# Optimization experiments

Measured on AMD Instinct MI355X. Metric: run time of the kernel, lower is better.

## Reference

```python
import jax, jax.numpy as jnp
import numpy as np

B, NS, D, H, L, NQ, NK = 32, 4096, 256, 4, 6, 512, 1024
DH = D // H
SCALE = 1.0 / np.sqrt(DH)


def _ln(x, scale, bias, eps=1e-5):
    m = jnp.mean(x, axis=-1, keepdims=True)
    v = jnp.mean((x - m) ** 2, axis=-1, keepdims=True)
    return (x - m) * jax.lax.rsqrt(v + eps) * scale + bias


def setup_inputs() -> dict:
    key = jax.random.key(0)
    ks = jax.random.split(key, 12)
    d = {
        'update_tensor': jax.random.normal(ks[0], (B, NS, D), jnp.float32) * 0.1,
        'emb_table': jax.random.normal(ks[1], (NS + 1, D), jnp.float32) * 0.1,
        'mask_logits': jax.random.uniform(ks[2], (L, NQ, NK), jnp.float32),
        'Wq': jax.random.normal(ks[3], (D, D), jnp.float32) * 0.05,
        'Wk': jax.random.normal(ks[4], (D, D), jnp.float32) * 0.05,
        'Wv': jax.random.normal(ks[5], (D, D), jnp.float32) * 0.05,
        'Wo': jax.random.normal(ks[6], (D, D), jnp.float32) * 0.05,
        'W1': jax.random.normal(ks[7], (D, D), jnp.float32) * 0.05,
        'b1': jnp.zeros((D,), jnp.float32),
        'W2': jax.random.normal(ks[8], (D, D), jnp.float32) * 0.05,
        'b2': jnp.zeros((D,), jnp.float32),
        'sys_scale': jnp.ones((D,), jnp.float32),
        'sys_bias': jnp.zeros((D,), jnp.float32),
        'eff_scale': jnp.ones((D,), jnp.float32),
        'eff_bias': jnp.zeros((D,), jnp.float32),
        'inner_scale': jnp.ones((D,), jnp.float32),
        'inner_bias': jnp.zeros((D,), jnp.float32),
        'outer_scale': jnp.ones((D,), jnp.float32),
        'outer_bias': jnp.zeros((D,), jnp.float32),
        'query_idx': jax.random.randint(ks[9], (L, NQ), 0, NS).astype(jnp.int32),
        'key_idx': jax.random.randint(ks[10], (L, NK), 0, NS).astype(jnp.int32),
    }
    return d


def _hitr(q, k, mask, Wq, Wk, Wv, Wo, W1, b1, W2, b2, in_s, in_b, out_s, out_b):
    # q: [B,NQ,D] (pre-normed), k: [B,NK,D], mask: [NQ,NK] bool
    Q = jnp.einsum('bqd,de->bqe', q, Wq).reshape(B, NQ, H, DH)
    K = jnp.einsum('bkd,de->bke', k, Wk).reshape(B, NK, H, DH)
    V = jnp.einsum('bkd,de->bke', k, Wv).reshape(B, NK, H, DH)
    scores = jnp.einsum('bqhd,bkhd->bhqk', Q, K) * SCALE
    scores = jnp.where(mask[None, None], scores, jnp.float32(-1e9))
    attn = jax.nn.softmax(scores, axis=-1)
    ctx = jnp.einsum('bhqk,bkhd->bqhd', attn, V).reshape(B, NQ, D)
    h = _ln(jnp.einsum('bqd,de->bqe', ctx, Wo), in_s, in_b)
    ffn = jnp.einsum('bqd,de->bqe', jax.nn.gelu(jnp.einsum('bqd,de->bqe', h, W1) + b1), W2) + b2
    return _ln(h + ffn, out_s, out_b)


def reference(update_tensor, emb_table, mask_logits, Wq, Wk, Wv, Wo, W1, b1, W2, b2,
              sys_scale, sys_bias, eff_scale, eff_bias, inner_scale, inner_bias,
              outer_scale, outer_bias, query_idx, key_idx):
    update_result = jnp.zeros_like(update_tensor)
    for l in range(L):  # static hierarchy levels
        qi, ki = query_idx[l], key_idx[l]
        mask = mask_logits[l] > 0.5
        q = _ln(emb_table[qi][None] + update_tensor[:, qi], sys_scale, sys_bias)
        k = _ln(emb_table[ki][None] + update_tensor[:, ki], sys_scale, sys_bias)
        res = _ln(_hitr(q, k, mask, Wq, Wk, Wv, Wo, W1, b1, W2, b2,
                        inner_scale, inner_bias, outer_scale, outer_bias),
                  eff_scale, eff_bias)
        update_tensor = update_tensor.at[:, qi].add(res)
        update_result = update_result.at[:, qi].add(res)
    return update_result
```

## Files before the change

kernel.cpp:

```cpp
#include <hip/hip_runtime.h>
#include <cstdint>
#include <cstddef>

#define B_ 32
#define NS_ 4096
#define D_ 256
#define H_ 4
#define L_ 6
#define NQ_ 512
#define NK_ 1024
#define DH_ 64
#define SCALE_ 0.125f

typedef unsigned short ushort_t;
typedef unsigned long long u64_t;
typedef __bf16 bf16x8 __attribute__((ext_vector_type(8)));
typedef float f32x4 __attribute__((ext_vector_type(4)));

__device__ __forceinline__ ushort_t f2bf(float f) {
  unsigned u = __float_as_uint(f);
  u += 0x7fffu + ((u >> 16) & 1u);
  return (ushort_t)(u >> 16);
}

__device__ __forceinline__ void gld16(const void* g, void* l) {
  __builtin_amdgcn_global_load_lds(
      (__attribute__((address_space(1))) void*)(uintptr_t)g,
      (__attribute__((address_space(3))) void*)(uintptr_t)l, 16, 0, 0);
}

__device__ __forceinline__ float2 block_sum2(float a, float b) {
  __shared__ float sA[4], sB[4];
#pragma unroll
  for (int o = 32; o; o >>= 1) {
    a += __shfl_xor(a, o);
    b += __shfl_xor(b, o);
  }
  const int w = threadIdx.x >> 6;
  __syncthreads();
  if ((threadIdx.x & 63) == 0) { sA[w] = a; sB[w] = b; }
  __syncthreads();
  return make_float2(sA[0] + sA[1] + sA[2] + sA[3], sB[0] + sB[1] + sB[2] + sB[3]);
}

__global__ __launch_bounds__(256) void prep_w(
    const float* __restrict__ w0, const float* __restrict__ w1,
    const float* __restrict__ w2, const float* __restrict__ w3,
    const float* __restrict__ w4, const float* __restrict__ w5,
    ushort_t* __restrict__ wt) {
  const int sel = blockIdx.x >> 8;
  const int n = blockIdx.x & 255;
  const int k = threadIdx.x;
  const float* W = sel == 0 ? w0 : sel == 1 ? w1 : sel == 2 ? w2
                 : sel == 3 ? w3 : sel == 4 ? w4 : w5;
  wt[sel * 65536 + n * 256 + k] = f2bf(W[k * 256 + n]);
}

__global__ __launch_bounds__(256) void prep_mask(
    const float* __restrict__ ml, u64_t* __restrict__ mb) {
  const long gid = (long)blockIdx.x * 256 + threadIdx.x;
  const bool m = ml[gid] > 0.5f;
  const u64_t bal = __ballot(m);
  if ((threadIdx.x & 63) == 0) mb[gid >> 6] = bal;
}

__global__ __launch_bounds__(256) void gather_ln(
    const float* __restrict__ ut, const float* __restrict__ emb,
    const int* __restrict__ qidx, const int* __restrict__ kidx,
    const float* __restrict__ sc, const float* __restrict__ bi,
    ushort_t* __restrict__ qn, ushort_t* __restrict__ kn) {
  const int r = blockIdx.x;
  const int t = threadIdx.x;
  int bb, idx;
  ushort_t* dst;
  long drow;
  if (r < B_ * NQ_) {
    bb = r >> 9; idx = qidx[r & (NQ_ - 1)]; dst = qn; drow = r;
  } else {
    const int r2 = r - B_ * NQ_;
    bb = r2 >> 10; idx = kidx[r2 & (NK_ - 1)]; dst = kn; drow = r2;
  }
  const float x = emb[(long)idx * 256 + t] + ut[((long)bb * NS_ + idx) * 256 + t];
  const float2 s = block_sum2(x, x * x);
  const float mean = s.x * (1.f / 256.f);
  const float var = s.y * (1.f / 256.f) - mean * mean;
  const float inv = rsqrtf(var + 1e-5f);
  dst[drow * 256 + t] = f2bf((x - mean) * inv * sc[t] + bi[t]);
}

template <int EPI>
__device__ __forceinline__ void gemm_body(
    const ushort_t* __restrict__ A, const ushort_t* __restrict__ Bt,
    const float* __restrict__ bias, void* __restrict__ Cout,
    long m0, int n0, ushort_t* lAB) {
  ushort_t* lA = lAB;
  ushort_t* lB = lAB + 8192;
  const int tid = threadIdx.x;
  const int lane = tid & 63, w = tid >> 6;
  const int quad = lane >> 4, l16 = lane & 15;
  const int wm = w & 1, wn = w >> 1;

  f32x4 acc[4][4] = {};

  for (int kt = 0; kt < 4; ++kt) {
    const int k0 = kt * 64;
#pragma unroll
    for (int p = 0; p < 4; ++p) {
      const int ob = p * 4096 + tid * 16;
      const int row = ob >> 7;
      const int chunk = ((ob >> 4) & 7) ^ (row & 7);
      gld16(A + (m0 + row) * 256 + k0 + chunk * 8, (char*)lA + p * 4096 + w * 1024);
      gld16(Bt + (long)(n0 + row) * 256 + k0 + chunk * 8, (char*)lB + p * 4096 + w * 1024);
    }
    __syncthreads();
#pragma unroll
    for (int ki = 0; ki < 2; ++ki) {
      bf16x8 af[4], bfr[4];
#pragma unroll
      for (int i = 0; i < 4; ++i) {
        const int ra = wm * 64 + i * 16 + l16;
        const int ca = (ki * 4 + quad) ^ (ra & 7);
        af[i] = *(const bf16x8*)&lA[ra * 64 + ca * 8];
        const int rb = wn * 64 + i * 16 + l16;
        const int cb = (ki * 4 + quad) ^ (rb & 7);
        bfr[i] = *(const bf16x8*)&lB[rb * 64 + cb * 8];
      }
#pragma unroll
      for (int mi = 0; mi < 4; ++mi)
#pragma unroll
        for (int ni = 0; ni < 4; ++ni)
          acc[mi][ni] = __builtin_amdgcn_mfma_f32_16x16x32_bf16(af[mi], bfr[ni], acc[mi][ni], 0, 0, 0);
    }
    __syncthreads();
  }

  if (EPI == 4) {
    const long b = m0 >> 10;
    const int kvseg = (int)(m0 & 1023);
#pragma unroll
    for (int hg = 0; hg < 2; ++hg) {
      if (wn == hg) {
#pragma unroll
        for (int mi = 0; mi < 4; ++mi)
#pragma unroll
          for (int ni = 0; ni < 4; ++ni)
#pragma unroll
            for (int r = 0; r < 4; ++r) {
              const int dh = ni * 16 + l16;
              const int kvl = wm * 64 + mi * 16 + quad * 4 + r;
              lAB[dh * 128 + (((kvl >> 3) ^ (dh & 15)) << 3) + (kvl & 7)] =
                  f2bf(acc[mi][ni][r]);
            }
      }
      __syncthreads();
      {
        const int dh = tid >> 2;
        const int head = (n0 >> 6) + hg;
        ushort_t* dst = (ushort_t*)Cout +
            ((b * 4 + head) * 64 + dh) * 1024 + kvseg;
#pragma unroll
        for (int i = 0; i < 4; ++i) {
          const int c = (tid & 3) * 4 + i;
          const int cs = c ^ (dh & 15);
          *(uint4*)(dst + c * 8) = *(const uint4*)&lAB[dh * 128 + cs * 8];
        }
      }
      __syncthreads();
    }
    return;
  }

#pragma unroll
  for (int mi = 0; mi < 4; ++mi) {
#pragma unroll
    for (int ni = 0; ni < 4; ++ni) {
#pragma unroll
      for (int r = 0; r < 4; ++r) {
        const long row = m0 + wm * 64 + mi * 16 + quad * 4 + r;
        const int col = n0 + wn * 64 + ni * 16 + l16;
        float v = acc[mi][ni][r];
        if (EPI == 2 || EPI == 3) v += bias[col];
        if (EPI == 2) {
          const float u = 0.7978845608028654f * (v + 0.044715f * v * v * v);
          v = 0.5f * v * (1.0f + tanhf(u));
        }
        if (EPI == 5) v *= SCALE_;
        if (EPI == 0 || EPI == 2 || EPI == 5)
          ((ushort_t*)Cout)[row * 256 + col] = f2bf(v);
        else
          ((float*)Cout)[row * 256 + col] = v;
      }
    }
  }
}

template <int EPI>
__global__ __launch_bounds__(256) void gemm256(
    const ushort_t* __restrict__ A, const ushort_t* __restrict__ Bt,
    const float* __restrict__ bias, void* __restrict__ Cout) {
  __shared__ ushort_t lAB[16384];
  gemm_body<EPI>(A, Bt, bias, Cout, (long)blockIdx.x * 128, blockIdx.y * 128, lAB);
}

__global__ __launch_bounds__(256) void gemm_qkv(
    const ushort_t* __restrict__ qn, const ushort_t* __restrict__ kn,
    const ushort_t* __restrict__ wt,
    ushort_t* __restrict__ Qb, ushort_t* __restrict__ Kb, ushort_t* __restrict__ Vt) {
  __shared__ ushort_t lAB[16384];
  int idx = blockIdx.x;
  if (idx < 256) {
    gemm_body<5>(qn, wt, nullptr, Qb, (long)(idx & 127) * 128, (idx >> 7) * 128, lAB);
  } else if (idx < 768) {
    idx -= 256;
    gemm_body<0>(kn, wt + 65536, nullptr, Kb, (long)(idx & 255) * 128, (idx >> 8) * 128, lAB);
  } else {
    idx -= 768;
    gemm_body<4>(kn, wt + 131072, nullptr, Vt, (long)(idx & 255) * 128, (idx >> 8) * 128, lAB);
  }
}

__global__ __launch_bounds__(256) void attn_kernel(
    const ushort_t* __restrict__ Qb, const ushort_t* __restrict__ Kb,
    const ushort_t* __restrict__ Vt, const u64_t* __restrict__ mbits,
    ushort_t* __restrict__ ctx) {
  __shared__ ushort_t lQ[4096], lK[4096], lVt[4096], lP[4096];
  const int tid = threadIdx.x;
  const int lane = tid & 63, w = tid >> 6;
  const int quad = lane >> 4, l16 = lane & 15;
  const int bid = blockIdx.x;
  const int qt = bid >> 7, pair = bid & 127;
  const int h = pair & 3, b = pair >> 2;
  const int q0 = qt * 64;
  const long qrow0 = (long)b * NQ_ + q0;
  const long krow0 = (long)b * NK_;
  const ushort_t* vbase = Vt + ((long)pair * 64) * 1024;
  const u64_t* mrow = mbits + (long)(q0 + w * 16 + quad * 4) * (NK_ / 64);

#pragma unroll
  for (int p = 0; p < 2; ++p) {
    const int ob = p * 4096 + tid * 16;
    const int row = ob >> 7;
    const int chunk = ((ob >> 4) & 7) ^ (row & 7);
    gld16(Qb + (qrow0 + row) * 256 + h * 64 + chunk * 8, (char*)lQ + p * 4096 + w * 1024);
    gld16(Kb + (krow0 + row) * 256 + h * 64 + chunk * 8, (char*)lK + p * 4096 + w * 1024);
  }

  f32x4 o_acc[4] = {};
  f32x4 l_acc = {};
  bf16x8 ones;
#pragma unroll
  for (int i = 0; i < 8; ++i) ones[i] = (__bf16)1.0f;

  u64_t wd[4];
#pragma unroll
  for (int r = 0; r < 4; ++r) wd[r] = mrow[r << 4];

  for (int kt = 0; kt < 16; ++kt) {
    __syncthreads();

#pragma unroll
    for (int p = 0; p < 2; ++p) {
      const int ob = p * 4096 + tid * 16;
      const int row = ob >> 7;
      const int chunk = ((ob >> 4) & 7) ^ (row & 7);
      gld16(vbase + (long)row * 1024 + kt * 64 + chunk * 8,
            (char*)lVt + p * 4096 + w * 1024);
    }

    f32x4 s[4] = {};
    __builtin_amdgcn_s_setprio(1);
#pragma unroll
    for (int ki = 0; ki < 2; ++ki) {
      const int rq = w * 16 + l16;
      const int cq = (ki * 4 + quad) ^ (rq & 7);
      const bf16x8 qf = *(const bf16x8*)&lQ[rq * 64 + cq * 8];
#pragma unroll
      for (int ni = 0; ni < 4; ++ni) {
        const int rk = ni * 16 + l16;
        const int ck = (ki * 4 + quad) ^ (rk & 7);
        const bf16x8 kf = *(const bf16x8*)&lK[rk * 64 + ck * 8];
        s[ni] = __builtin_amdgcn_mfma_f32_16x16x32_bf16(qf, kf, s[ni], 0, 0, 0);
      }
    }
    __builtin_amdgcn_s_setprio(0);

    u64_t wdn[4];
    if (kt < 15) {
#pragma unroll
      for (int r = 0; r < 4; ++r) wdn[r] = mrow[(r << 4) + kt + 1];
    }

#pragma unroll
    for (int r = 0; r < 4; ++r) {
      const int rowp = w * 16 + quad * 4 + r;
#pragma unroll
      for (int ni = 0; ni < 4; ++ni) {
        const bool keep = (wd[r] >> (ni * 16 + l16)) & 1ull;
        const float pv = keep ? __expf(s[ni][r]) : 0.f;
        const int col = ni * 16 + l16;
        lP[rowp * 64 + (((col >> 3) ^ (rowp & 7)) << 3) + (col & 7)] = f2bf(pv);
      }
    }
    if (kt < 15) {
#pragma unroll
      for (int r = 0; r < 4; ++r) wd[r] = wdn[r];
    }

    __syncthreads();

    if (kt < 15) {
#pragma unroll
      for (int p = 0; p < 2; ++p) {
        const int ob = p * 4096 + tid * 16;
        const int row = ob >> 7;
        const int chunk = ((ob >> 4) & 7) ^ (row & 7);
        gld16(Kb + (krow0 + (kt + 1) * 64 + row) * 256 + h * 64 + chunk * 8,
              (char*)lK + p * 4096 + w * 1024);
      }
    }

    __builtin_amdgcn_s_setprio(1);
#pragma unroll
    for (int ki = 0; ki < 2; ++ki) {
      const int rp = w * 16 + l16;
      const int cp = (ki * 4 + quad) ^ (rp & 7);
      const bf16x8 pf = *(const bf16x8*)&lP[rp * 64 + cp * 8];
      l_acc = __builtin_amdgcn_mfma_f32_16x16x32_bf16(pf, ones, l_acc, 0, 0, 0);
#pragma unroll
      for (int ni = 0; ni < 4; ++ni) {
        const int rv = ni * 16 + l16;
        const int cv = (ki * 4 + quad) ^ (rv & 7);
        const bf16x8 vf = *(const bf16x8*)&lVt[rv * 64 + cv * 8];
        o_acc[ni] = __builtin_amdgcn_mfma_f32_16x16x32_bf16(pf, vf, o_acc[ni], 0, 0, 0);
      }
    }
    __builtin_amdgcn_s_setprio(0);
  }

#pragma unroll
  for (int r = 0; r < 4; ++r) {
    const float inv = 1.0f / l_acc[r];
    const long rowg = qrow0 + w * 16 + quad * 4 + r;
#pragma unroll
    for (int ni = 0; ni < 4; ++ni) {
      const int col = h * 64 + ni * 16 + l16;
      ctx[rowg * 256 + col] = f2bf(o_acc[ni][r] * inv);
    }
  }
}

__global__ __launch_bounds__(256) void ln_inner(
    const float* __restrict__ in, const float* __restrict__ sc,
    const float* __restrict__ bi, float* __restrict__ of,
    ushort_t* __restrict__ ob) {
  const long r = blockIdx.x;
  const int t = threadIdx.x;
  const float x = in[r * 256 + t];
  const float2 s = block_sum2(x, x * x);
  const float mean = s.x * (1.f / 256.f);
  const float inv = rsqrtf(s.y * (1.f / 256.f) - mean * mean + 1e-5f);
  const float y = (x - mean) * inv * sc[t] + bi[t];
  of[r * 256 + t] = y;
  ob[r * 256 + t] = f2bf(y);
}

__global__ __launch_bounds__(256) void final_scatter(
    const float* __restrict__ h, const float* __restrict__ ffn,
    const float* __restrict__ osc, const float* __restrict__ obi,
    const float* __restrict__ esc, const float* __restrict__ ebi,
    const int* __restrict__ qidx, float* __restrict__ ut,
    float* __restrict__ out) {
  const int r = blockIdx.x;
  const int t = threadIdx.x;
  const float x = h[(long)r * 256 + t] + ffn[(long)r * 256 + t];
  float2 s = block_sum2(x, x * x);
  float mean = s.x * (1.f / 256.f);
  float inv = rsqrtf(s.y * (1.f / 256.f) - mean * mean + 1e-5f);
  const float y = (x - mean) * inv * osc[t] + obi[t];
  s = block_sum2(y, y * y);
  mean = s.x * (1.f / 256.f);
  inv = rsqrtf(s.y * (1.f / 256.f) - mean * mean + 1e-5f);
  const float z = (y - mean) * inv * esc[t] + ebi[t];
  const int idx = qidx[r & (NQ_ - 1)];
  const int bb = r >> 9;
  const long off = ((long)bb * NS_ + idx) * 256 + t;
  atomicAdd(&ut[off], z);
  atomicAdd(&out[off], z);
}

extern "C" void kernel_launch(void* const* d_in, const int* in_sizes, int n_in,
                              void* d_out, int out_size, void* d_ws, size_t ws_size,
                              hipStream_t stream) {
  float* ut = (float*)d_in[0];
  const float* emb = (const float*)d_in[1];
  const float* maskl = (const float*)d_in[2];
  const float* Wq = (const float*)d_in[3];
  const float* Wk = (const float*)d_in[4];
  const float* Wv = (const float*)d_in[5];
  const float* Wo = (const float*)d_in[6];
  const float* W1 = (const float*)d_in[7];
  const float* b1 = (const float*)d_in[8];
  const float* W2 = (const float*)d_in[9];
  const float* b2 = (const float*)d_in[10];
  const float* sys_s = (const float*)d_in[11];
  const float* sys_b = (const float*)d_in[12];
  const float* eff_s = (const float*)d_in[13];
  const float* eff_b = (const float*)d_in[14];
  const float* in_s = (const float*)d_in[15];
  const float* in_b = (const float*)d_in[16];
  const float* out_s = (const float*)d_in[17];
  const float* out_b = (const float*)d_in[18];
  const int* qidx = (const int*)d_in[19];
  const int* kidx = (const int*)d_in[20];
  float* out = (float*)d_out;

  char* p = (char*)d_ws;
  auto carve = [&](size_t bytes) {
    void* r = (void*)p;
    p += (bytes + 255) & ~(size_t)255;
    return r;
  };
  ushort_t* wt = (ushort_t*)carve((size_t)6 * 65536 * 2);
  u64_t* mb = (u64_t*)carve((size_t)L_ * NQ_ * (NK_ / 64) * 8);
  ushort_t* qn = (ushort_t*)carve((size_t)16384 * 256 * 2);
  ushort_t* kn = (ushort_t*)carve((size_t)32768 * 256 * 2);
  ushort_t* Qb = (ushort_t*)carve((size_t)16384 * 256 * 2);
  ushort_t* Kb = (ushort_t*)carve((size_t)32768 * 256 * 2);
  ushort_t* Vt = (ushort_t*)carve((size_t)32768 * 256 * 2);
  float* hraw = (float*)carve((size_t)16384 * 256 * 4);

  ushort_t* ctx = qn;
  ushort_t* g = Qb;
  ushort_t* hb = Kb;
  float* hf = (float*)Vt;
  float* ffn = hraw;

  hipMemsetAsync(d_out, 0, (size_t)out_size, stream);
  prep_w<<<1536, 256, 0, stream>>>(Wq, Wk, Wv, Wo, W1, W2, wt);
  prep_mask<<<(L_ * NQ_ * NK_) / 256, 256, 0, stream>>>(maskl, mb);

  for (int l = 0; l < L_; ++l) {
    gather_ln<<<B_ * (NQ_ + NK_), 256, 0, stream>>>(
        ut, emb, qidx + l * NQ_, kidx + l * NK_, sys_s, sys_b, qn, kn);
    gemm_qkv<<<1280, 256, 0, stream>>>(qn, kn, wt, Qb, Kb, Vt);
    attn_kernel<<<1024, 256, 0, stream>>>(
        Qb, Kb, Vt, mb + (size_t)l * NQ_ * (NK_ / 64), ctx);
    gemm256<1><<<dim3(128, 2), 256, 0, stream>>>(ctx, wt + 3 * 65536, nullptr, hraw);
    ln_inner<<<16384, 256, 0, stream>>>(hraw, in_s, in_b, hf, hb);
    gemm256<2><<<dim3(128, 2), 256, 0, stream>>>(hb, wt + 4 * 65536, b1, g);
    gemm256<3><<<dim3(128, 2), 256, 0, stream>>>(g, wt + 5 * 65536, b2, ffn);
    final_scatter<<<16384, 256, 0, stream>>>(
        hf, ffn, out_s, out_b, eff_s, eff_b, qidx + l * NQ_, ut, out);
  }
}
```

Before: 1.378 ms.

## Fuse layernorms and scatter into full-row output GEMM epilogues

```diff
diff --git a/kernel.cpp b/kernel.cpp
--- a/kernel.cpp
+++ b/kernel.cpp
@@ -91,8 +91,7 @@
 template <int EPI>
 __device__ __forceinline__ void gemm_body(
     const ushort_t* __restrict__ A, const ushort_t* __restrict__ Bt,
-    const float* __restrict__ bias, void* __restrict__ Cout,
-    long m0, int n0, ushort_t* lAB) {
+    void* __restrict__ Cout, long m0, int n0, ushort_t* lAB) {
   ushort_t* lA = lAB;
   ushort_t* lB = lAB + 8192;
   const int tid = threadIdx.x;
@@ -179,27 +178,11 @@
         const long row = m0 + wm * 64 + mi * 16 + quad * 4 + r;
         const int col = n0 + wn * 64 + ni * 16 + l16;
         float v = acc[mi][ni][r];
-        if (EPI == 2 || EPI == 3) v += bias[col];
-        if (EPI == 2) {
-          const float u = 0.7978845608028654f * (v + 0.044715f * v * v * v);
-          v = 0.5f * v * (1.0f + tanhf(u));
-        }
         if (EPI == 5) v *= SCALE_;
-        if (EPI == 0 || EPI == 2 || EPI == 5)
-          ((ushort_t*)Cout)[row * 256 + col] = f2bf(v);
-        else
-          ((float*)Cout)[row * 256 + col] = v;
-      }
-    }
-  }
-}
-
-template <int EPI>
-__global__ __launch_bounds__(256) void gemm256(
-    const ushort_t* __restrict__ A, const ushort_t* __restrict__ Bt,
-    const float* __restrict__ bias, void* __restrict__ Cout) {
-  __shared__ ushort_t lAB[16384];
-  gemm_body<EPI>(A, Bt, bias, Cout, (long)blockIdx.x * 128, blockIdx.y * 128, lAB);
+        ((ushort_t*)Cout)[row * 256 + col] = f2bf(v);
+      }
+    }
+  }
 }
 
 __global__ __launch_bounds__(256) void gemm_qkv(
@@ -209,13 +192,141 @@
   __shared__ ushort_t lAB[16384];
   int idx = blockIdx.x;
   if (idx < 256) {
-    gemm_body<5>(qn, wt, nullptr, Qb, (long)(idx & 127) * 128, (idx >> 7) * 128, lAB);
+    gemm_body<5>(qn, wt, Qb, (long)(idx & 127) * 128, (idx >> 7) * 128, lAB);
   } else if (idx < 768) {
     idx -= 256;
-    gemm_body<0>(kn, wt + 65536, nullptr, Kb, (long)(idx & 255) * 128, (idx >> 8) * 128, lAB);
+    gemm_body<0>(kn, wt + 65536, Kb, (long)(idx & 255) * 128, (idx >> 8) * 128, lAB);
   } else {
     idx -= 768;
-    gemm_body<4>(kn, wt + 131072, nullptr, Vt, (long)(idx & 255) * 128, (idx >> 8) * 128, lAB);
+    gemm_body<4>(kn, wt + 131072, Vt, (long)(idx & 255) * 128, (idx >> 8) * 128, lAB);
+  }
+}
+
+template <int MODE>
+__global__ __launch_bounds__(256) void gemm_row(
+    const ushort_t* __restrict__ A, const ushort_t* __restrict__ Bt,
+    const float* __restrict__ bias,
+    const float* __restrict__ ln1s, const float* __restrict__ ln1b,
+    const float* __restrict__ ln2s, const float* __restrict__ ln2b,
+    const float* __restrict__ hfres, const int* __restrict__ qidx,
+    float* __restrict__ outF, ushort_t* __restrict__ outB,
+    float* __restrict__ ut, float* __restrict__ out) {
+  __shared__ ushort_t lA[4096];
+  __shared__ ushort_t lB[16384];
+  const int tid = threadIdx.x;
+  const int lane = tid & 63, w = tid >> 6;
+  const int quad = lane >> 4, l16 = lane & 15;
+  const long m0 = (long)blockIdx.x * 64;
+
+  f32x4 acc[16] = {};
+
+  for (int kt = 0; kt < 4; ++kt) {
+    const int k0 = kt * 64;
+#pragma unroll
+    for (int p = 0; p < 2; ++p) {
+      const int ob = p * 4096 + tid * 16;
+      const int row = ob >> 7;
+      const int chunk = ((ob >> 4) & 7) ^ (row & 7);
+      gld16(A + (m0 + row) * 256 + k0 + chunk * 8, (char*)lA + p * 4096 + w * 1024);
+    }
+#pragma unroll
+    for (int p = 0; p < 8; ++p) {
+      const int ob = p * 4096 + tid * 16;
+      const int row = ob >> 7;
+      const int chunk = ((ob >> 4) & 7) ^ (row & 7);
+      gld16(Bt + (long)row * 256 + k0 + chunk * 8, (char*)lB + p * 4096 + w * 1024);
+    }
+    __syncthreads();
+#pragma unroll
+    for (int ki = 0; ki < 2; ++ki) {
+      const int ra = w * 16 + l16;
+      const int ca = (ki * 4 + quad) ^ (ra & 7);
+      const bf16x8 af = *(const bf16x8*)&lA[ra * 64 + ca * 8];
+#pragma unroll
+      for (int ni = 0; ni < 16; ++ni) {
+        const int rb = ni * 16 + l16;
+        const int cb = (ki * 4 + quad) ^ (rb & 7);
+        const bf16x8 bfr = *(const bf16x8*)&lB[rb * 64 + cb * 8];
+        acc[ni] = __builtin_amdgcn_mfma_f32_16x16x32_bf16(af, bfr, acc[ni], 0, 0, 0);
+      }
+    }
+    __syncthreads();
+  }
+
+#pragma unroll
+  for (int r = 0; r < 4; ++r) {
+    const long row = m0 + w * 16 + quad * 4 + r;
+    if (MODE == 2) {
+#pragma unroll
+      for (int ni = 0; ni < 16; ++ni) {
+        const int col = ni * 16 + l16;
+        float v = acc[ni][r] + bias[col];
+        const float u = 0.7978845608028654f * (v + 0.044715f * v * v * v);
+        v = 0.5f * v * (1.0f + tanhf(u));
+        outB[row * 256 + col] = f2bf(v);
+      }
+    } else if (MODE == 6) {
+      float s1 = 0.f, s2 = 0.f;
+#pragma unroll
+      for (int ni = 0; ni < 16; ++ni) {
+        const float v = acc[ni][r];
+        s1 += v; s2 += v * v;
+      }
+#pragma unroll
+      for (int off = 1; off < 16; off <<= 1) {
+        s1 += __shfl_xor(s1, off);
+        s2 += __shfl_xor(s2, off);
+      }
+      const float mean = s1 * (1.f / 256.f);
+      const float inv = rsqrtf(s2 * (1.f / 256.f) - mean * mean + 1e-5f);
+#pragma unroll
+      for (int ni = 0; ni < 16; ++ni) {
+        const int col = ni * 16 + l16;
+        const float y = (acc[ni][r] - mean) * inv * ln1s[col] + ln1b[col];
+        outF[row * 256 + col] = y;
+        outB[row * 256 + col] = f2bf(y);
+      }
+    } else {
+      float x[16];
+      float s1 = 0.f, s2 = 0.f;
+#pragma unroll
+      for (int ni = 0; ni < 16; ++ni) {
+        const int col = ni * 16 + l16;
+        const float v = acc[ni][r] + bias[col] + hfres[row * 256 + col];
+        x[ni] = v; s1 += v; s2 += v * v;
+      }
+#pragma unroll
+      for (int off = 1; off < 16; off <<= 1) {
+        s1 += __shfl_xor(s1, off);
+        s2 += __shfl_xor(s2, off);
+      }
+      float mean = s1 * (1.f / 256.f);
+      float inv = rsqrtf(s2 * (1.f / 256.f) - mean * mean + 1e-5f);
+      float y[16];
+      s1 = 0.f; s2 = 0.f;
+#pragma unroll
+      for (int ni = 0; ni < 16; ++ni) {
+        const int col = ni * 16 + l16;
+        const float v = (x[ni] - mean) * inv * ln1s[col] + ln1b[col];
+        y[ni] = v; s1 += v; s2 += v * v;
+      }
+#pragma unroll
+      for (int off = 1; off < 16; off <<= 1) {
+        s1 += __shfl_xor(s1, off);
+        s2 += __shfl_xor(s2, off);
+      }
+      mean = s1 * (1.f / 256.f);
+      inv = rsqrtf(s2 * (1.f / 256.f) - mean * mean + 1e-5f);
+      const int idx = qidx[(int)(row & (NQ_ - 1))];
+      const long base = ((row >> 9) * (long)NS_ + idx) * 256;
+#pragma unroll
+      for (int ni = 0; ni < 16; ++ni) {
+        const int col = ni * 16 + l16;
+        const float z = (y[ni] - mean) * inv * ln2s[col] + ln2b[col];
+        atomicAdd(&ut[base + col], z);
+        atomicAdd(&out[base + col], z);
+      }
+    }
   }
 }
 
@@ -347,45 +458,6 @@
       ctx[rowg * 256 + col] = f2bf(o_acc[ni][r] * inv);
     }
   }
-}
-
-__global__ __launch_bounds__(256) void ln_inner(
-    const float* __restrict__ in, const float* __restrict__ sc,
-    const float* __restrict__ bi, float* __restrict__ of,
-    ushort_t* __restrict__ ob) {
-  const long r = blockIdx.x;
-  const int t = threadIdx.x;
-  const float x = in[r * 256 + t];
-  const float2 s = block_sum2(x, x * x);
-  const float mean = s.x * (1.f / 256.f);
-  const float inv = rsqrtf(s.y * (1.f / 256.f) - mean * mean + 1e-5f);
-  const float y = (x - mean) * inv * sc[t] + bi[t];
-  of[r * 256 + t] = y;
-  ob[r * 256 + t] = f2bf(y);
-}
-
-__global__ __launch_bounds__(256) void final_scatter(
-    const float* __restrict__ h, const float* __restrict__ ffn,
-    const float* __restrict__ osc, const float* __restrict__ obi,
-    const float* __restrict__ esc, const float* __restrict__ ebi,
-    const int* __restrict__ qidx, float* __restrict__ ut,
-    float* __restrict__ out) {
-  const int r = blockIdx.x;
-  const int t = threadIdx.x;
-  const float x = h[(long)r * 256 + t] + ffn[(long)r * 256 + t];
-  float2 s = block_sum2(x, x * x);
-  float mean = s.x * (1.f / 256.f);
-  float inv = rsqrtf(s.y * (1.f / 256.f) - mean * mean + 1e-5f);
-  const float y = (x - mean) * inv * osc[t] + obi[t];
-  s = block_sum2(y, y * y);
-  mean = s.x * (1.f / 256.f);
-  inv = rsqrtf(s.y * (1.f / 256.f) - mean * mean + 1e-5f);
-  const float z = (y - mean) * inv * esc[t] + ebi[t];
-  const int idx = qidx[r & (NQ_ - 1)];
-  const int bb = r >> 9;
-  const long off = ((long)bb * NS_ + idx) * 256 + t;
-  atomicAdd(&ut[off], z);
-  atomicAdd(&out[off], z);
 }
 
 extern "C" void kernel_launch(void* const* d_in, const int* in_sizes, int n_in,
@@ -427,13 +499,11 @@
   ushort_t* Qb = (ushort_t*)carve((size_t)16384 * 256 * 2);
   ushort_t* Kb = (ushort_t*)carve((size_t)32768 * 256 * 2);
   ushort_t* Vt = (ushort_t*)carve((size_t)32768 * 256 * 2);
-  float* hraw = (float*)carve((size_t)16384 * 256 * 4);
 
   ushort_t* ctx = qn;
   ushort_t* g = Qb;
   ushort_t* hb = Kb;
   float* hf = (float*)Vt;
-  float* ffn = hraw;
 
   hipMemsetAsync(d_out, 0, (size_t)out_size, stream);
   prep_w<<<1536, 256, 0, stream>>>(Wq, Wk, Wv, Wo, W1, W2, wt);
@@ -445,11 +515,14 @@
     gemm_qkv<<<1280, 256, 0, stream>>>(qn, kn, wt, Qb, Kb, Vt);
     attn_kernel<<<1024, 256, 0, stream>>>(
         Qb, Kb, Vt, mb + (size_t)l * NQ_ * (NK_ / 64), ctx);
-    gemm256<1><<<dim3(128, 2), 256, 0, stream>>>(ctx, wt + 3 * 65536, nullptr, hraw);
-    ln_inner<<<16384, 256, 0, stream>>>(hraw, in_s, in_b, hf, hb);
-    gemm256<2><<<dim3(128, 2), 256, 0, stream>>>(hb, wt + 4 * 65536, b1, g);
-    gemm256<3><<<dim3(128, 2), 256, 0, stream>>>(g, wt + 5 * 65536, b2, ffn);
-    final_scatter<<<16384, 256, 0, stream>>>(
-        hf, ffn, out_s, out_b, eff_s, eff_b, qidx + l * NQ_, ut, out);
-  }
-}
+    gemm_row<6><<<256, 256, 0, stream>>>(
+        ctx, wt + 3 * 65536, nullptr, in_s, in_b, nullptr, nullptr,
+        nullptr, nullptr, hf, hb, nullptr, nullptr);
+    gemm_row<2><<<256, 256, 0, stream>>>(
+        hb, wt + 4 * 65536, b1, nullptr, nullptr, nullptr, nullptr,
+        nullptr, nullptr, nullptr, g, nullptr, nullptr);
+    gemm_row<7><<<256, 256, 0, stream>>>(
+        g, wt + 5 * 65536, b2, out_s, out_b, eff_s, eff_b,
+        hf, qidx + l * NQ_, nullptr, nullptr, ut, out);
+  }
+}
```

Result: slower. 1.556 ms (+13.0%).
